# Optimization experiments

Measured on AMD Instinct MI355X. Metric: run time of the kernel, lower is better.

Reference implementation:

```python
import jax, jax.numpy as jnp
import numpy as np

M, NQ, NKV, DX, DT = 8, 1024, 1024, 512, 2
H, HD = 8, 64            # num_heads, head_dim
INNER = H * HD           # 512
KHID = 16                # kernel MLP hidden dim
SCALE = HD ** -0.5


def setup_inputs() -> dict:
    key = jax.random.key(0)
    ks = jax.random.split(key, 16)
    s = lambda fan_in: 1.0 / np.sqrt(fan_in)
    return {
        "xq": jax.random.normal(ks[0], (M, NQ, DX), jnp.float32),
        "xk": jax.random.normal(ks[1], (M, NKV, DX), jnp.float32),
        "xv": jax.random.normal(ks[2], (M, NKV, DX), jnp.float32),
        "tq": jax.random.normal(ks[3], (M, NQ, DT), jnp.float32),
        "tk": jax.random.normal(ks[4], (M, NKV, DT), jnp.float32),
        # attention projections (bias=False for q/k/v, Linear bias for out)
        "w_q": jax.random.normal(ks[5], (DX, INNER), jnp.float32) * s(DX),
        "w_k": jax.random.normal(ks[6], (DX, INNER), jnp.float32) * s(DX),
        "w_v": jax.random.normal(ks[7], (DX, INNER), jnp.float32) * s(DX),
        "w_out": jax.random.normal(ks[8], (INNER, DX), jnp.float32) * s(INNER),
        "b_out": jnp.zeros((DX,), jnp.float32),
        # kernel MLP: dt -> KHID -> H (per-head pairwise bias)
        "kw1": jax.random.normal(ks[9], (DT, KHID), jnp.float32) * s(DT),
        "kb1": jnp.zeros((KHID,), jnp.float32),
        "kw2": jax.random.normal(ks[10], (KHID, H), jnp.float32) * s(KHID),
        "kb2": jnp.zeros((H,), jnp.float32),
    }


def reference(xq, xk, xv, tq, tk, w_q, w_k, w_v, w_out, b_out, kw1, kb1, kw2, kb2):
    # pairwise differences of input locations: [m, nq, nkv, dt]
    diff = tq[:, :, None, :] - tk[:, None, :, :]
    # kernel MLP -> per-head bias, rearranged to [m, h, nq, nkv]
    hmid = jax.nn.relu(diff @ kw1 + kb1)          # [m, nq, nkv, KHID]
    dots = jnp.einsum('mqkc,ch->mhqk', hmid, kw2) + kb2[None, :, None, None]
    # token attention: standard scaled QK scores
    q = (xq @ w_q).reshape(M, NQ, H, HD)          # [m, nq, h, d]
    k = (xk @ w_k).reshape(M, NKV, H, HD)
    token_dots = jnp.einsum('mqhd,mkhd->mhqk', q, k) * SCALE
    dots = dots + token_dots
    attn = jax.nn.softmax(dots, axis=-1)          # softmax over keys
    v = (xv @ w_v).reshape(M, NKV, H, HD)
    out = jnp.einsum('mhqk,mkhd->mqhd', attn, v).reshape(M, NQ, INNER)
    return out @ w_out + b_out                    # [m, nq, dx]
```

## Files before the change

### kernel.cpp

```cpp
#include <hip/hip_runtime.h>


typedef unsigned short u16;
typedef unsigned int   u32;
typedef short bf8 __attribute__((ext_vector_type(8)));
typedef float f4  __attribute__((ext_vector_type(4)));

#define Mb 8
#define SCALE 0.125f

__device__ __forceinline__ u16 f2bf(float f) {
    union { float f; u32 u; } v; v.f = f;
    u32 r = v.u + 0x7fffu + ((v.u >> 16) & 1u);
    return (u16)(r >> 16);
}
__device__ __forceinline__ u32 pk2(float a, float b) {
    return (u32)f2bf(a) | ((u32)f2bf(b) << 16);
}

struct GArgs {
    const void*  A[3];
    const float* W[3];
    void*        C[3];
    const float* bias;
    int          modeT[3];
    int          outf32;
    int          abf16;
};

__global__ __launch_bounds__(256) void gemm_mfma(GArgs g) {
    __shared__ u16 Xs[4][128][8];
    __shared__ u16 Ws[4][128][8];

    const int z   = blockIdx.z;
    const int tid = threadIdx.x;
    const int w = tid >> 6, lane = tid & 63, quad = lane >> 4, l16 = lane & 15;
    const int wm = w >> 1, wn = w & 1;
    const int n0 = blockIdx.x * 128, t0 = blockIdx.y * 128;
    const int trans = g.modeT[z];

    f4 acc[4][4];
    #pragma unroll
    for (int i = 0; i < 4; ++i)
        #pragma unroll
        for (int j = 0; j < 4; ++j) acc[i][j] = (f4)0.f;

    const float* Wp = g.W[z];

    for (int kc = 0; kc < 512; kc += 32) {
        __syncthreads();
        {
            const int row = tid >> 1, half = tid & 1;
            if (g.abf16) {
                const u16* ap = (const u16*)g.A[z] + (size_t)(t0 + row) * 512 + kc + half * 16;
                uint4 v0 = *(const uint4*)ap;
                uint4 v1 = *(const uint4*)(ap + 8);
                *(uint4*)&Xs[half * 2][row][0]     = v0;
                *(uint4*)&Xs[half * 2 + 1][row][0] = v1;
            } else {
                const float* ap = (const float*)g.A[z] + (size_t)(t0 + row) * 512 + kc + half * 16;
                float4 a0 = *(const float4*)(ap + 0);
                float4 a1 = *(const float4*)(ap + 4);
                float4 a2 = *(const float4*)(ap + 8);
                float4 a3 = *(const float4*)(ap + 12);
                uint4 v0, v1;
                v0.x = pk2(a0.x, a0.y); v0.y = pk2(a0.z, a0.w);
                v0.z = pk2(a1.x, a1.y); v0.w = pk2(a1.z, a1.w);
                v1.x = pk2(a2.x, a2.y); v1.y = pk2(a2.z, a2.w);
                v1.z = pk2(a3.x, a3.y); v1.w = pk2(a3.z, a3.w);
                *(uint4*)&Xs[half * 2][row][0]     = v0;
                *(uint4*)&Xs[half * 2 + 1][row][0] = v1;
            }
        }
        #pragma unroll
        for (int i = 0; i < 4; ++i) {
            const int s = tid + i * 256;
            const int n = s & 127, kg = s >> 7;
            const int kb = kc + kg * 4;
            float v0 = Wp[(size_t)(kb + 0) * 512 + n0 + n];
            float v1 = Wp[(size_t)(kb + 1) * 512 + n0 + n];
            float v2 = Wp[(size_t)(kb + 2) * 512 + n0 + n];
            float v3 = Wp[(size_t)(kb + 3) * 512 + n0 + n];
            uint2 pw; pw.x = pk2(v0, v1); pw.y = pk2(v2, v3);
            *(uint2*)&Ws[kg >> 1][n][(kg & 1) * 4] = pw;
        }
        __syncthreads();

        const u16 (*Aop)[128][8] = trans ? Xs : Ws;
        const u16 (*Bop)[128][8] = trans ? Ws : Xs;
        const int arow = (trans ? wm : wn) * 64;
        const int brow = (trans ? wn : wm) * 64;
        bf8 af[4], bf[4];
        #pragma unroll
        for (int i = 0; i < 4; ++i) af[i] = *(const bf8*)&Aop[quad][arow + i * 16 + l16][0];
        #pragma unroll
        for (int j = 0; j < 4; ++j) bf[j] = *(const bf8*)&Bop[quad][brow + j * 16 + l16][0];
        #pragma unroll
        for (int i = 0; i < 4; ++i)
            #pragma unroll
            for (int j = 0; j < 4; ++j)
                acc[i][j] = __builtin_amdgcn_mfma_f32_16x16x32_bf16(af[i], bf[j], acc[i][j], 0, 0, 0);
    }

    if (g.outf32) {
        float* Co = (float*)g.C[z];
        #pragma unroll
        for (int i = 0; i < 4; ++i) {
            const int nb = n0 + wn * 64 + i * 16 + quad * 4;
            float4 bv = *(const float4*)&g.bias[nb];
            #pragma unroll
            for (int j = 0; j < 4; ++j) {
                const int tok = t0 + wm * 64 + j * 16 + l16;
                float4 st;
                st.x = acc[i][j][0] + bv.x; st.y = acc[i][j][1] + bv.y;
                st.z = acc[i][j][2] + bv.z; st.w = acc[i][j][3] + bv.w;
                *(float4*)&Co[(size_t)tok * 512 + nb] = st;
            }
        }
    } else if (!trans) {
        u16* C = (u16*)g.C[z];
        #pragma unroll
        for (int i = 0; i < 4; ++i) {
            const int nb = n0 + wn * 64 + i * 16 + quad * 4;
            #pragma unroll
            for (int j = 0; j < 4; ++j) {
                const int tok = t0 + wm * 64 + j * 16 + l16;
                uint2 pw;
                pw.x = pk2(acc[i][j][0], acc[i][j][1]);
                pw.y = pk2(acc[i][j][2], acc[i][j][3]);
                *(uint2*)&C[(size_t)tok * 512 + nb] = pw;
            }
        }
    } else {
        u16* Vt = (u16*)g.C[z];
        #pragma unroll
        for (int i = 0; i < 4; ++i) {
            const int tokb = t0 + wm * 64 + i * 16 + quad * 4;
            const int mb = tokb >> 10, tb = tokb & 1023;
            #pragma unroll
            for (int j = 0; j < 4; ++j) {
                const int n = n0 + wn * 64 + j * 16 + l16;
                uint2 pw;
                pw.x = pk2(acc[i][j][0], acc[i][j][1]);
                pw.y = pk2(acc[i][j][2], acc[i][j][3]);
                *(uint2*)&Vt[(size_t)mb * 524288 + (size_t)n * 1024 + tb] = pw;
            }
        }
    }
}

__global__ __launch_bounds__(256) void attn_mfma(
    const u16* __restrict__ Q, const u16* __restrict__ K,
    const u16* __restrict__ Vt,
    const float* __restrict__ tqp, const float* __restrict__ tkp,
    const float* __restrict__ kw1, const float* __restrict__ kb1,
    const float* __restrict__ kw2,
    u16* __restrict__ O)
{
    __shared__ u16   sK[8][64][8];
    __shared__ u16   sV[8][64][8];
    __shared__ float sv[16][68];
    __shared__ u16   sP[4][16][68];

    const int tid = threadIdx.x;
    const int w = tid >> 6, lane = tid & 63, quad = lane >> 4, l16 = lane & 15;
    const int qt = blockIdx.x, h = blockIdx.y, m = blockIdx.z;
    const int q0 = qt * 64;
    const size_t qtok = (size_t)m * 1024 + q0 + w * 16 + l16;

    bf8 qf[2];
    {
        const u16* qp = Q + qtok * 512 + h * 64 + quad * 8;
        qf[0] = *(const bf8*)qp;
        qf[1] = *(const bf8*)(qp + 32);
    }
    float u[16], w2h[16];
    {
        const float t0v = tqp[qtok * 2], t1v = tqp[qtok * 2 + 1];
        #pragma unroll
        for (int c = 0; c < 16; ++c) {
            u[c] = fmaf(t0v, kw1[c], fmaf(t1v, kw1[16 + c], kb1[c]));
            w2h[c] = kw2[c * 8 + h];
        }
    }

    float mrun = -1e30f, lrun = 0.f;
    f4 o[4];
    #pragma unroll
    for (int d = 0; d < 4; ++d) o[d] = (f4)0.f;

    for (int kt = 0; kt < 16; ++kt) {
        const int k0 = kt * 64;
        __syncthreads();
        #pragma unroll
        for (int i = 0; i < 2; ++i) {
            const int s = tid + i * 256;
            const int seg = s >> 6, key = s & 63;
            const u16* kp = K + ((size_t)m * 1024 + k0 + key) * 512 + h * 64 + seg * 8;
            *(uint4*)&sK[seg][key][0] = *(const uint4*)kp;
        }
        #pragma unroll
        for (int i = 0; i < 2; ++i) {
            const int s = tid + i * 256;
            const int ks = s >> 6, d = s & 63;
            const u16* vp = Vt + (size_t)m * 524288 + (size_t)(h * 64 + d) * 1024 + k0 + ks * 8;
            *(uint4*)&sV[ks][d][0] = *(const uint4*)vp;
        }
        {
            const int c = tid >> 4, k4 = (tid & 15) * 4;
            const float* tkq = tkp + ((size_t)m * 1024 + k0 + k4) * 2;
            float4 ta = *(const float4*)tkq;
            float4 tb = *(const float4*)(tkq + 4);
            const float w0 = kw1[c], w1 = kw1[16 + c];
            float4 vv;
            vv.x = fmaf(ta.x, w0, ta.y * w1);
            vv.y = fmaf(ta.z, w0, ta.w * w1);
            vv.z = fmaf(tb.x, w0, tb.y * w1);
            vv.w = fmaf(tb.z, w0, tb.w * w1);
            *(float4*)&sv[c][k4] = vv;
        }
        __syncthreads();

        f4 s[4];
        #pragma unroll
        for (int msub = 0; msub < 4; ++msub) {
            bf8 kf0 = *(const bf8*)&sK[quad][msub * 16 + l16][0];
            bf8 kf1 = *(const bf8*)&sK[4 + quad][msub * 16 + l16][0];
            s[msub] = __builtin_amdgcn_mfma_f32_16x16x32_bf16(kf0, qf[0], (f4)0.f, 0, 0, 0);
            s[msub] = __builtin_amdgcn_mfma_f32_16x16x32_bf16(kf1, qf[1], s[msub], 0, 0, 0);
        }
        #pragma unroll
        for (int msub = 0; msub < 4; ++msub) {
            const int kb = msub * 16 + quad * 4;
            f4 b = (f4)0.f;
            #pragma unroll
            for (int c = 0; c < 16; ++c) {
                float4 vv = *(const float4*)&sv[c][kb];
                const float uc = u[c], wc = w2h[c];
                b[0] = fmaf(fmaxf(uc - vv.x, 0.f), wc, b[0]);
                b[1] = fmaf(fmaxf(uc - vv.y, 0.f), wc, b[1]);
                b[2] = fmaf(fmaxf(uc - vv.z, 0.f), wc, b[2]);
                b[3] = fmaf(fmaxf(uc - vv.w, 0.f), wc, b[3]);
            }
            s[msub] = s[msub] * SCALE + b;
        }
        float mx = -1e30f;
        #pragma unroll
        for (int msub = 0; msub < 4; ++msub) {
            mx = fmaxf(mx, fmaxf(fmaxf(s[msub][0], s[msub][1]),
                                 fmaxf(s[msub][2], s[msub][3])));
        }
        mx = fmaxf(mx, __shfl_xor(mx, 16));
        mx = fmaxf(mx, __shfl_xor(mx, 32));
        const float mnew = fmaxf(mrun, mx);
        const float alpha = __expf(mrun - mnew);
        float ps = 0.f;
        #pragma unroll
        for (int msub = 0; msub < 4; ++msub) {
            #pragma unroll
            for (int r = 0; r < 4; ++r) {
                float p = __expf(s[msub][r] - mnew);
                s[msub][r] = p;
                ps += p;
            }
        }
        ps += __shfl_xor(ps, 16);
        ps += __shfl_xor(ps, 32);
        lrun = lrun * alpha + ps;
        mrun = mnew;
        #pragma unroll
        for (int d = 0; d < 4; ++d) o[d] = o[d] * alpha;
        #pragma unroll
        for (int msub = 0; msub < 4; ++msub) {
            uint2 pw;
            pw.x = pk2(s[msub][0], s[msub][1]);
            pw.y = pk2(s[msub][2], s[msub][3]);
            *(uint2*)&sP[w][l16][msub * 16 + quad * 4] = pw;
        }
        #pragma unroll
        for (int dsub = 0; dsub < 4; ++dsub) {
            #pragma unroll
            for (int kc2 = 0; kc2 < 2; ++kc2) {
                bf8 vf = *(const bf8*)&sV[kc2 * 4 + quad][dsub * 16 + l16][0];
                bf8 pf = *(const bf8*)&sP[w][l16][kc2 * 32 + quad * 8];
                o[dsub] = __builtin_amdgcn_mfma_f32_16x16x32_bf16(vf, pf, o[dsub], 0, 0, 0);
            }
        }
    }

    const float inv = 1.f / lrun;
    #pragma unroll
    for (int dsub = 0; dsub < 4; ++dsub) {
        uint2 pw;
        pw.x = pk2(o[dsub][0] * inv, o[dsub][1] * inv);
        pw.y = pk2(o[dsub][2] * inv, o[dsub][3] * inv);
        *(uint2*)&O[qtok * 512 + h * 64 + dsub * 16 + quad * 4] = pw;
    }
}

extern "C" void kernel_launch(void* const* d_in, const int* in_sizes, int n_in,
                              void* d_out, int out_size, void* d_ws, size_t ws_size,
                              hipStream_t stream) {
    const float* xq    = (const float*)d_in[0];
    const float* xk    = (const float*)d_in[1];
    const float* xv    = (const float*)d_in[2];
    const float* tq    = (const float*)d_in[3];
    const float* tk    = (const float*)d_in[4];
    const float* w_q   = (const float*)d_in[5];
    const float* w_k   = (const float*)d_in[6];
    const float* w_v   = (const float*)d_in[7];
    const float* w_out = (const float*)d_in[8];
    const float* b_out = (const float*)d_in[9];
    const float* kw1   = (const float*)d_in[10];
    const float* kb1   = (const float*)d_in[11];
    const float* kw2   = (const float*)d_in[12];

    const size_t nTok = (size_t)Mb * 1024 * 512;
    u16* Q  = (u16*)d_ws;
    u16* Kp = Q + nTok;
    u16* Vt = Kp + nTok;
    u16* O  = Vt + nTok;

    GArgs gq;
    gq.A[0] = xq;  gq.A[1] = xk;  gq.A[2] = xv;
    gq.W[0] = w_q; gq.W[1] = w_k; gq.W[2] = w_v;
    gq.C[0] = Q;   gq.C[1] = Kp;  gq.C[2] = Vt;
    gq.bias = nullptr;
    gq.modeT[0] = 0; gq.modeT[1] = 0; gq.modeT[2] = 1;
    gq.outf32 = 0; gq.abf16 = 0;
    gemm_mfma<<<dim3(4, 64, 3), 256, 0, stream>>>(gq);

    attn_mfma<<<dim3(16, 8, Mb), 256, 0, stream>>>(Q, Kp, Vt, tq, tk,
                                                   kw1, kb1, kw2, O);

    GArgs go;
    go.A[0] = O;     go.A[1] = O;     go.A[2] = O;
    go.W[0] = w_out; go.W[1] = w_out; go.W[2] = w_out;
    go.C[0] = d_out; go.C[1] = d_out; go.C[2] = d_out;
    go.bias = b_out;
    go.modeT[0] = 0; go.modeT[1] = 0; go.modeT[2] = 0;
    go.outf32 = 1; go.abf16 = 1;
    gemm_mfma<<<dim3(4, 64, 1), 256, 0, stream>>>(go);
}
```

Before: 307.3 us.

## Restructure attention: all heads per block, MFMA kernel-MLP bias, pre-transposed bf16 weights

Adds a weight-conversion kernel that transposes and casts all four projection weights to bf16 once per call, so the GEMM loads weight tiles with wide contiguous reads instead of strided fp32 loads. The attention kernel is rebuilt so one 512-thread block handles all 8 heads for 32 queries. The pairwise kernel-MLP bias is computed once per key tile with an MFMA and shared across heads through LDS, rather than being recomputed with scalar FMAs in every head block. K and V now go straight from global memory into registers without LDS staging. This trades an extra launch and workspace for less redundant bias work and cheaper weight loads, but the direct K/V loads and smaller key tiles may lower memory efficiency.

```diff
diff --git a/kernel.cpp b/kernel.cpp
--- a/kernel.cpp
+++ b/kernel.cpp
@@ -18,14 +18,42 @@
     return (u32)f2bf(a) | ((u32)f2bf(b) << 16);
 }
 
+__global__ __launch_bounds__(256) void wconv(
+    const float* __restrict__ w0, const float* __restrict__ w1,
+    const float* __restrict__ w2, const float* __restrict__ w3,
+    u16* __restrict__ o0, u16* __restrict__ o1,
+    u16* __restrict__ o2, u16* __restrict__ o3)
+{
+    const float* W[4] = {w0, w1, w2, w3};
+    u16*         O[4] = {o0, o1, o2, o3};
+    __shared__ float L[64][65];
+    const int z = blockIdx.z, tid = threadIdx.x;
+    const int k0 = blockIdx.x * 64, n0 = blockIdx.y * 64;
+    const float* Wz = W[z];
+    #pragma unroll
+    for (int i = 0; i < 16; ++i) {
+        int idx = tid + i * 256;
+        int k = idx >> 6, n = idx & 63;
+        L[n][k] = Wz[(size_t)(k0 + k) * 512 + n0 + n];
+    }
+    __syncthreads();
+    u32* Oz = (u32*)O[z];
+    #pragma unroll
+    for (int i = 0; i < 8; ++i) {
+        int idx = tid + i * 256;
+        int n = idx >> 5, kp = idx & 31;
+        Oz[((size_t)(n0 + n) * 512 + k0 + kp * 2) >> 1] = pk2(L[n][kp * 2], L[n][kp * 2 + 1]);
+    }
+}
+
 struct GArgs {
-    const void*  A[3];
-    const float* W[3];
-    void*        C[3];
+    const void* A[3];
+    const u16*  W[3];
+    void*       C[3];
     const float* bias;
-    int          modeT[3];
-    int          outf32;
-    int          abf16;
+    int modeT[3];
+    int outf32;
+    int abf16;
 };
 
 __global__ __launch_bounds__(256) void gemm_mfma(GArgs g) {
@@ -45,44 +73,33 @@
         #pragma unroll
         for (int j = 0; j < 4; ++j) acc[i][j] = (f4)0.f;
 
-    const float* Wp = g.W[z];
+    const u16* Wp = g.W[z];
 
     for (int kc = 0; kc < 512; kc += 32) {
         __syncthreads();
-        {
-            const int row = tid >> 1, half = tid & 1;
+        #pragma unroll
+        for (int i = 0; i < 2; ++i) {
+            const int cc = tid + i * 256;
+            const int row = cc >> 2, seg = cc & 3;
             if (g.abf16) {
-                const u16* ap = (const u16*)g.A[z] + (size_t)(t0 + row) * 512 + kc + half * 16;
-                uint4 v0 = *(const uint4*)ap;
-                uint4 v1 = *(const uint4*)(ap + 8);
-                *(uint4*)&Xs[half * 2][row][0]     = v0;
-                *(uint4*)&Xs[half * 2 + 1][row][0] = v1;
+                const u16* ap = (const u16*)g.A[z] + (size_t)(t0 + row) * 512 + kc + seg * 8;
+                *(uint4*)&Xs[seg][row][0] = *(const uint4*)ap;
             } else {
-                const float* ap = (const float*)g.A[z] + (size_t)(t0 + row) * 512 + kc + half * 16;
-                float4 a0 = *(const float4*)(ap + 0);
+                const float* ap = (const float*)g.A[z] + (size_t)(t0 + row) * 512 + kc + seg * 8;
+                float4 a0 = *(const float4*)ap;
                 float4 a1 = *(const float4*)(ap + 4);
-                float4 a2 = *(const float4*)(ap + 8);
-                float4 a3 = *(const float4*)(ap + 12);
-                uint4 v0, v1;
-                v0.x = pk2(a0.x, a0.y); v0.y = pk2(a0.z, a0.w);
-                v0.z = pk2(a1.x, a1.y); v0.w = pk2(a1.z, a1.w);
-                v1.x = pk2(a2.x, a2.y); v1.y = pk2(a2.z, a2.w);
-                v1.z = pk2(a3.x, a3.y); v1.w = pk2(a3.z, a3.w);
-                *(uint4*)&Xs[half * 2][row][0]     = v0;
-                *(uint4*)&Xs[half * 2 + 1][row][0] = v1;
-            }
-        }
-        #pragma unroll
-        for (int i = 0; i < 4; ++i) {
-            const int s = tid + i * 256;
-            const int n = s & 127, kg = s >> 7;
-            const int kb = kc + kg * 4;
-            float v0 = Wp[(size_t)(kb + 0) * 512 + n0 + n];
-            float v1 = Wp[(size_t)(kb + 1) * 512 + n0 + n];
-            float v2 = Wp[(size_t)(kb + 2) * 512 + n0 + n];
-            float v3 = Wp[(size_t)(kb + 3) * 512 + n0 + n];
-            uint2 pw; pw.x = pk2(v0, v1); pw.y = pk2(v2, v3);
-            *(uint2*)&Ws[kg >> 1][n][(kg & 1) * 4] = pw;
+                uint4 v;
+                v.x = pk2(a0.x, a0.y); v.y = pk2(a0.z, a0.w);
+                v.z = pk2(a1.x, a1.y); v.w = pk2(a1.z, a1.w);
+                *(uint4*)&Xs[seg][row][0] = v;
+            }
+        }
+        #pragma unroll
+        for (int i = 0; i < 2; ++i) {
+            const int cc = tid + i * 256;
+            const int row = cc >> 2, seg = cc & 3;
+            const u16* bp = Wp + (size_t)(n0 + row) * 512 + kc + seg * 8;
+            *(uint4*)&Ws[seg][row][0] = *(const uint4*)bp;
         }
         __syncthreads();
 
@@ -149,7 +166,7 @@
     }
 }
 
-__global__ __launch_bounds__(256) void attn_mfma(
+__global__ __launch_bounds__(512) void attn_mfma(
     const u16* __restrict__ Q, const u16* __restrict__ K,
     const u16* __restrict__ Vt,
     const float* __restrict__ tqp, const float* __restrict__ tkp,
@@ -157,144 +174,169 @@
     const float* __restrict__ kw2,
     u16* __restrict__ O)
 {
-    __shared__ u16   sK[8][64][8];
-    __shared__ u16   sV[8][64][8];
-    __shared__ float sv[16][68];
-    __shared__ u16   sP[4][16][68];
+    __shared__ float sv[32][20];
+    __shared__ float sB[32][9][33];
+    __shared__ u16   sP[8][32][40];
 
     const int tid = threadIdx.x;
     const int w = tid >> 6, lane = tid & 63, quad = lane >> 4, l16 = lane & 15;
-    const int qt = blockIdx.x, h = blockIdx.y, m = blockIdx.z;
-    const int q0 = qt * 64;
-    const size_t qtok = (size_t)m * 1024 + q0 + w * 16 + l16;
-
-    bf8 qf[2];
+    const int m = blockIdx.x;
+    const int q0 = blockIdx.y * 32;
+    const int h = w;
+
+    bf8 qf[2][2];
+    #pragma unroll
+    for (int qs = 0; qs < 2; ++qs)
+        #pragma unroll
+        for (int kc = 0; kc < 2; ++kc)
+            qf[qs][kc] = *(const bf8*)(Q + ((size_t)m * 1024 + q0 + qs * 16 + l16) * 512
+                                         + h * 64 + kc * 32 + quad * 8);
+    float u[2][8];
     {
-        const u16* qp = Q + qtok * 512 + h * 64 + quad * 8;
-        qf[0] = *(const bf8*)qp;
-        qf[1] = *(const bf8*)(qp + 32);
-    }
-    float u[16], w2h[16];
+        #pragma unroll
+        for (int qs = 0; qs < 2; ++qs) {
+            const size_t qi = ((size_t)m * 1024 + q0 + qs * 16 + l16) * 2;
+            const float t0v = tqp[qi], t1v = tqp[qi + 1];
+            #pragma unroll
+            for (int j = 0; j < 8; ++j) {
+                const int c = (quad & 1) * 8 + j;
+                u[qs][j] = fmaf(t0v, kw1[c], fmaf(t1v, kw1[16 + c], kb1[c]));
+            }
+        }
+    }
+    bf8 b2;
     {
-        const float t0v = tqp[qtok * 2], t1v = tqp[qtok * 2 + 1];
-        #pragma unroll
-        for (int c = 0; c < 16; ++c) {
-            u[c] = fmaf(t0v, kw1[c], fmaf(t1v, kw1[16 + c], kb1[c]));
-            w2h[c] = kw2[c * 8 + h];
-        }
-    }
-
-    float mrun = -1e30f, lrun = 0.f;
-    f4 o[4];
-    #pragma unroll
-    for (int d = 0; d < 4; ++d) o[d] = (f4)0.f;
-
-    for (int kt = 0; kt < 16; ++kt) {
-        const int k0 = kt * 64;
+        union { uint4 u4; bf8 v; } cv; cv.u4 = make_uint4(0, 0, 0, 0);
+        if (l16 < 8 && quad < 2) {
+            u32 r[4];
+            #pragma unroll
+            for (int p = 0; p < 4; ++p) {
+                const int c = quad * 8 + p * 2;
+                r[p] = pk2(kw2[c * 8 + l16], kw2[(c + 1) * 8 + l16]);
+            }
+            cv.u4 = make_uint4(r[0], r[1], r[2], r[3]);
+        }
+        b2 = cv.v;
+    }
+    const int svk = tid >> 4, svc = tid & 15;
+    const float svw0 = kw1[svc], svw1 = kw1[16 + svc];
+
+    float mrun[2] = {-1e30f, -1e30f}, lrun[2] = {0.f, 0.f};
+    f4 o[2][4];
+    #pragma unroll
+    for (int qs = 0; qs < 2; ++qs)
+        #pragma unroll
+        for (int d = 0; d < 4; ++d) o[qs][d] = (f4)0.f;
+
+    for (int kt = 0; kt < 32; ++kt) {
+        const int k0 = kt * 32;
+
+        bf8 kf[2][2], vf[4];
+        #pragma unroll
+        for (int ms = 0; ms < 2; ++ms)
+            #pragma unroll
+            for (int kc = 0; kc < 2; ++kc)
+                kf[ms][kc] = *(const bf8*)(K + ((size_t)m * 1024 + k0 + ms * 16 + l16) * 512
+                                             + h * 64 + kc * 32 + quad * 8);
+        #pragma unroll
+        for (int ds = 0; ds < 4; ++ds)
+            vf[ds] = *(const bf8*)(Vt + (size_t)m * 524288
+                                      + (size_t)(h * 64 + ds * 16 + l16) * 1024 + k0 + quad * 8);
+
+        {
+            const size_t ki = ((size_t)m * 1024 + k0 + svk) * 2;
+            const float t0v = tkp[ki], t1v = tkp[ki + 1];
+            sv[svk][svc] = fmaf(t0v, svw0, t1v * svw1);
+        }
         __syncthreads();
-        #pragma unroll
-        for (int i = 0; i < 2; ++i) {
-            const int s = tid + i * 256;
-            const int seg = s >> 6, key = s & 63;
-            const u16* kp = K + ((size_t)m * 1024 + k0 + key) * 512 + h * 64 + seg * 8;
-            *(uint4*)&sK[seg][key][0] = *(const uint4*)kp;
-        }
-        #pragma unroll
-        for (int i = 0; i < 2; ++i) {
-            const int s = tid + i * 256;
-            const int ks = s >> 6, d = s & 63;
-            const u16* vp = Vt + (size_t)m * 524288 + (size_t)(h * 64 + d) * 1024 + k0 + ks * 8;
-            *(uint4*)&sV[ks][d][0] = *(const uint4*)vp;
-        }
-        {
-            const int c = tid >> 4, k4 = (tid & 15) * 4;
-            const float* tkq = tkp + ((size_t)m * 1024 + k0 + k4) * 2;
-            float4 ta = *(const float4*)tkq;
-            float4 tb = *(const float4*)(tkq + 4);
-            const float w0 = kw1[c], w1 = kw1[16 + c];
-            float4 vv;
-            vv.x = fmaf(ta.x, w0, ta.y * w1);
-            vv.y = fmaf(ta.z, w0, ta.w * w1);
-            vv.z = fmaf(tb.x, w0, tb.y * w1);
-            vv.w = fmaf(tb.z, w0, tb.w * w1);
-            *(float4*)&sv[c][k4] = vv;
+
+        #pragma unroll
+        for (int tl = 0; tl < 4; ++tl) {
+            const int t = w * 4 + tl;
+            float4 v0, v1;
+            if (quad < 2) {
+                v0 = *(const float4*)&sv[t][quad * 8];
+                v1 = *(const float4*)&sv[t][quad * 8 + 4];
+            }
+            #pragma unroll
+            for (int qs = 0; qs < 2; ++qs) {
+                union { uint4 u4; bf8 v; } cv; cv.u4 = make_uint4(0, 0, 0, 0);
+                if (quad < 2) {
+                    cv.u4.x = pk2(fmaxf(u[qs][0] - v0.x, 0.f), fmaxf(u[qs][1] - v0.y, 0.f));
+                    cv.u4.y = pk2(fmaxf(u[qs][2] - v0.z, 0.f), fmaxf(u[qs][3] - v0.w, 0.f));
+                    cv.u4.z = pk2(fmaxf(u[qs][4] - v1.x, 0.f), fmaxf(u[qs][5] - v1.y, 0.f));
+                    cv.u4.w = pk2(fmaxf(u[qs][6] - v1.z, 0.f), fmaxf(u[qs][7] - v1.w, 0.f));
+                }
+                f4 d = __builtin_amdgcn_mfma_f32_16x16x32_bf16(cv.v, b2, (f4)0.f, 0, 0, 0);
+                if (l16 < 8) {
+                    #pragma unroll
+                    for (int r = 0; r < 4; ++r)
+                        sB[t][l16][qs * 16 + quad * 4 + r] = d[r];
+                }
+            }
         }
         __syncthreads();
 
-        f4 s[4];
-        #pragma unroll
-        for (int msub = 0; msub < 4; ++msub) {
-            bf8 kf0 = *(const bf8*)&sK[quad][msub * 16 + l16][0];
-            bf8 kf1 = *(const bf8*)&sK[4 + quad][msub * 16 + l16][0];
-            s[msub] = __builtin_amdgcn_mfma_f32_16x16x32_bf16(kf0, qf[0], (f4)0.f, 0, 0, 0);
-            s[msub] = __builtin_amdgcn_mfma_f32_16x16x32_bf16(kf1, qf[1], s[msub], 0, 0, 0);
-        }
-        #pragma unroll
-        for (int msub = 0; msub < 4; ++msub) {
-            const int kb = msub * 16 + quad * 4;
-            f4 b = (f4)0.f;
-            #pragma unroll
-            for (int c = 0; c < 16; ++c) {
-                float4 vv = *(const float4*)&sv[c][kb];
-                const float uc = u[c], wc = w2h[c];
-                b[0] = fmaf(fmaxf(uc - vv.x, 0.f), wc, b[0]);
-                b[1] = fmaf(fmaxf(uc - vv.y, 0.f), wc, b[1]);
-                b[2] = fmaf(fmaxf(uc - vv.z, 0.f), wc, b[2]);
-                b[3] = fmaf(fmaxf(uc - vv.w, 0.f), wc, b[3]);
-            }
-            s[msub] = s[msub] * SCALE + b;
-        }
-        float mx = -1e30f;
-        #pragma unroll
-        for (int msub = 0; msub < 4; ++msub) {
-            mx = fmaxf(mx, fmaxf(fmaxf(s[msub][0], s[msub][1]),
-                                 fmaxf(s[msub][2], s[msub][3])));
-        }
-        mx = fmaxf(mx, __shfl_xor(mx, 16));
-        mx = fmaxf(mx, __shfl_xor(mx, 32));
-        const float mnew = fmaxf(mrun, mx);
-        const float alpha = __expf(mrun - mnew);
-        float ps = 0.f;
-        #pragma unroll
-        for (int msub = 0; msub < 4; ++msub) {
-            #pragma unroll
-            for (int r = 0; r < 4; ++r) {
-                float p = __expf(s[msub][r] - mnew);
-                s[msub][r] = p;
-                ps += p;
-            }
-        }
-        ps += __shfl_xor(ps, 16);
-        ps += __shfl_xor(ps, 32);
-        lrun = lrun * alpha + ps;
-        mrun = mnew;
-        #pragma unroll
-        for (int d = 0; d < 4; ++d) o[d] = o[d] * alpha;
-        #pragma unroll
-        for (int msub = 0; msub < 4; ++msub) {
+        #pragma unroll
+        for (int qs = 0; qs < 2; ++qs) {
+            f4 s[2];
+            #pragma unroll
+            for (int ms = 0; ms < 2; ++ms) {
+                s[ms] = __builtin_amdgcn_mfma_f32_16x16x32_bf16(kf[ms][0], qf[qs][0], (f4)0.f, 0, 0, 0);
+                s[ms] = __builtin_amdgcn_mfma_f32_16x16x32_bf16(kf[ms][1], qf[qs][1], s[ms], 0, 0, 0);
+            }
+            #pragma unroll
+            for (int ms = 0; ms < 2; ++ms)
+                #pragma unroll
+                for (int r = 0; r < 4; ++r)
+                    s[ms][r] = fmaf(s[ms][r], SCALE,
+                                    sB[ms * 16 + quad * 4 + r][h][qs * 16 + l16]);
+            float mx = fmaxf(fmaxf(fmaxf(s[0][0], s[0][1]), fmaxf(s[0][2], s[0][3])),
+                             fmaxf(fmaxf(s[1][0], s[1][1]), fmaxf(s[1][2], s[1][3])));
+            mx = fmaxf(mx, __shfl_xor(mx, 16));
+            mx = fmaxf(mx, __shfl_xor(mx, 32));
+            const float mnew = fmaxf(mrun[qs], mx);
+            const float alpha = __expf(mrun[qs] - mnew);
+            float ps = 0.f;
+            #pragma unroll
+            for (int ms = 0; ms < 2; ++ms)
+                #pragma unroll
+                for (int r = 0; r < 4; ++r) {
+                    float p = __expf(s[ms][r] - mnew);
+                    s[ms][r] = p;
+                    ps += p;
+                }
+            ps += __shfl_xor(ps, 16);
+            ps += __shfl_xor(ps, 32);
+            lrun[qs] = lrun[qs] * alpha + ps;
+            mrun[qs] = mnew;
+            #pragma unroll
+            for (int ds = 0; ds < 4; ++ds) o[qs][ds] = o[qs][ds] * alpha;
+            #pragma unroll
+            for (int ms = 0; ms < 2; ++ms) {
+                uint2 pw;
+                pw.x = pk2(s[ms][0], s[ms][1]);
+                pw.y = pk2(s[ms][2], s[ms][3]);
+                *(uint2*)&sP[w][qs * 16 + l16][ms * 16 + quad * 4] = pw;
+            }
+            bf8 pf = *(const bf8*)&sP[w][qs * 16 + l16][quad * 8];
+            #pragma unroll
+            for (int ds = 0; ds < 4; ++ds)
+                o[qs][ds] = __builtin_amdgcn_mfma_f32_16x16x32_bf16(vf[ds], pf, o[qs][ds], 0, 0, 0);
+        }
+    }
+
+    #pragma unroll
+    for (int qs = 0; qs < 2; ++qs) {
+        const float inv = 1.f / lrun[qs];
+        u16* og = O + ((size_t)m * 1024 + q0 + qs * 16 + l16) * 512 + h * 64;
+        #pragma unroll
+        for (int ds = 0; ds < 4; ++ds) {
             uint2 pw;
-            pw.x = pk2(s[msub][0], s[msub][1]);
-            pw.y = pk2(s[msub][2], s[msub][3]);
-            *(uint2*)&sP[w][l16][msub * 16 + quad * 4] = pw;
-        }
-        #pragma unroll
-        for (int dsub = 0; dsub < 4; ++dsub) {
-            #pragma unroll
-            for (int kc2 = 0; kc2 < 2; ++kc2) {
-                bf8 vf = *(const bf8*)&sV[kc2 * 4 + quad][dsub * 16 + l16][0];
-                bf8 pf = *(const bf8*)&sP[w][l16][kc2 * 32 + quad * 8];
-                o[dsub] = __builtin_amdgcn_mfma_f32_16x16x32_bf16(vf, pf, o[dsub], 0, 0, 0);
-            }
-        }
-    }
-
-    const float inv = 1.f / lrun;
-    #pragma unroll
-    for (int dsub = 0; dsub < 4; ++dsub) {
-        uint2 pw;
-        pw.x = pk2(o[dsub][0] * inv, o[dsub][1] * inv);
-        pw.y = pk2(o[dsub][2] * inv, o[dsub][3] * inv);
-        *(uint2*)&O[qtok * 512 + h * 64 + dsub * 16 + quad * 4] = pw;
+            pw.x = pk2(o[qs][ds][0] * inv, o[qs][ds][1] * inv);
+            pw.y = pk2(o[qs][ds][2] * inv, o[qs][ds][3] * inv);
+            *(uint2*)(og + ds * 16 + quad * 4) = pw;
+        }
     }
 }
 
@@ -316,26 +358,31 @@
     const float* kw2   = (const float*)d_in[12];
 
     const size_t nTok = (size_t)Mb * 1024 * 512;
-    u16* Q  = (u16*)d_ws;
-    u16* Kp = Q + nTok;
-    u16* Vt = Kp + nTok;
-    u16* O  = Vt + nTok;
+    u16* Q   = (u16*)d_ws;
+    u16* Kp  = Q + nTok;
+    u16* Vt  = Kp + nTok;
+    u16* O   = Vt + nTok;
+    u16* Wt0 = O + nTok;
+    u16* Wt1 = Wt0 + 512 * 512;
+    u16* Wt2 = Wt1 + 512 * 512;
+    u16* Wt3 = Wt2 + 512 * 512;
+
+    wconv<<<dim3(8, 8, 4), 256, 0, stream>>>(w_q, w_k, w_v, w_out, Wt0, Wt1, Wt2, Wt3);
 
     GArgs gq;
     gq.A[0] = xq;  gq.A[1] = xk;  gq.A[2] = xv;
-    gq.W[0] = w_q; gq.W[1] = w_k; gq.W[2] = w_v;
+    gq.W[0] = Wt0; gq.W[1] = Wt1; gq.W[2] = Wt2;
     gq.C[0] = Q;   gq.C[1] = Kp;  gq.C[2] = Vt;
     gq.bias = nullptr;
     gq.modeT[0] = 0; gq.modeT[1] = 0; gq.modeT[2] = 1;
     gq.outf32 = 0; gq.abf16 = 0;
     gemm_mfma<<<dim3(4, 64, 3), 256, 0, stream>>>(gq);
 
-    attn_mfma<<<dim3(16, 8, Mb), 256, 0, stream>>>(Q, Kp, Vt, tq, tk,
-                                                   kw1, kb1, kw2, O);
+    attn_mfma<<<dim3(8, 32), 512, 0, stream>>>(Q, Kp, Vt, tq, tk, kw1, kb1, kw2, O);
 
     GArgs go;
-    go.A[0] = O;     go.A[1] = O;     go.A[2] = O;
-    go.W[0] = w_out; go.W[1] = w_out; go.W[2] = w_out;
+    go.A[0] = O;   go.A[1] = O;   go.A[2] = O;
+    go.W[0] = Wt3; go.W[1] = Wt3; go.W[2] = Wt3;
     go.C[0] = d_out; go.C[1] = d_out; go.C[2] = d_out;
     go.bias = b_out;
     go.modeT[0] = 0; go.modeT[1] = 0; go.modeT[2] = 0;
```

Measured after the change: 309.5 us. About the same (+0.7%).
